# Performance work log

Measured on AMD Instinct MI355X. Metric: run time of the kernel, lower is better.

Reference implementation:

```python
import jax, jax.numpy as jnp
import numpy as np

B, CQ, CKV, H, W = 16, 512, 512, 48, 48
NH = 8
HD = CQ // NH
SCALE = HD ** -0.5


def setup_inputs() -> dict:
    key = jax.random.key(0)
    ks = jax.random.split(key, 11)
    s = 0.02
    return {
        "query_features": jax.random.normal(ks[0], (B, CQ, H, W), jnp.float32),
        "key_features": jax.random.normal(ks[1], (B, CKV, H, W), jnp.float32),
        "value_features": jax.random.normal(ks[2], (B, CKV, H, W), jnp.float32),
        "Wq": jax.random.normal(ks[3], (CQ, CQ), jnp.float32) * s,
        "bq": jnp.zeros((CQ,), jnp.float32),
        "Wk": jax.random.normal(ks[4], (CQ, CKV), jnp.float32) * s,
        "bk": jnp.zeros((CQ,), jnp.float32),
        "Wv": jax.random.normal(ks[5], (CQ, CKV), jnp.float32) * s,
        "bv": jnp.zeros((CQ,), jnp.float32),
        "Wo": jax.random.normal(ks[6], (CQ, CQ), jnp.float32) * s,
        "bo": jnp.zeros((CQ,), jnp.float32),
    }


def _proj(x, Wt, b):
    # 1x1 conv == channel GEMM: (O,C) x (B,C,H,W) -> (B,O,H,W)
    return jnp.einsum('oc,bchw->bohw', Wt, x) + b[None, :, None, None]


def reference(query_features, key_features, value_features,
              Wq, bq, Wk, bk, Wv, bv, Wo, bo):
    b, cq, h, w = query_features.shape
    hw = h * w
    Q = _proj(query_features, Wq, bq).reshape(b, NH, HD, hw)
    K = _proj(key_features, Wk, bk).reshape(b, NH, HD, hw)
    V = _proj(value_features, Wv, bv).reshape(b, NH, HD, hw)
    # NOTE: faithful to source — contraction is over the SPATIAL axis d=H*W,
    # so scores are (B, NH, HD, HD) (head_dim x head_dim attention).
    scores = jnp.einsum('bnhd,bnkd->bnhk', Q, K) * SCALE
    attn = jax.nn.softmax(scores, axis=-1)
    out = jnp.einsum('bnhk,bnkd->bnhd', attn, V)  # (B, NH, HD, HW)
    out = out.reshape(b, cq, h, w)
    return _proj(out, Wo, bo)
```

## Files before the change

### kernel.cpp

```cpp
#include <hip/hip_runtime.h>
#include <hip/hip_bf16.h>

#define B_   16
#define C_   512
#define HW_  2304
#define NH_  8
#define HD_  64
#define SCALE_ 0.125f

typedef __bf16 bf16x8 __attribute__((ext_vector_type(8)));
typedef __bf16 bf16x4 __attribute__((ext_vector_type(4)));
typedef float  f32x4  __attribute__((ext_vector_type(4)));

#define MFMA16(a, b, c) __builtin_amdgcn_mfma_f32_16x16x32_bf16((a), (b), (c), 0, 0, 0)

__device__ __forceinline__ void gload_lds16(const void* g, void* l) {
    __builtin_amdgcn_global_load_lds(
        (const __attribute__((address_space(1))) unsigned int*)g,
        (__attribute__((address_space(3))) unsigned int*)l, 16, 0, 0);
}

__global__ __launch_bounds__(256) void prep(
    const float* __restrict__ X, __bf16* __restrict__ XT,
    const float* __restrict__ W, __bf16* __restrict__ Wb)
{
    const int t = threadIdx.x;
    if (blockIdx.z == 16) {
        const int bid = blockIdx.y * 18 + blockIdx.x;
        if (bid < 128) {
            const int idx = bid * 2048 + t * 8;
            const float4 f0 = *(const float4*)&W[idx];
            const float4 f1 = *(const float4*)&W[idx + 4];
            bf16x8 o;
            o[0] = (__bf16)f0.x; o[1] = (__bf16)f0.y; o[2] = (__bf16)f0.z; o[3] = (__bf16)f0.w;
            o[4] = (__bf16)f1.x; o[5] = (__bf16)f1.y; o[6] = (__bf16)f1.z; o[7] = (__bf16)f1.w;
            *(bf16x8*)&Wb[idx] = o;
        }
        return;
    }
    const int b  = blockIdx.z;
    const int c0 = blockIdx.y * 64;
    const int h0 = blockIdx.x * 128;
    const float* Xb = X + (size_t)b * C_ * HW_;
    __bf16* XTb = XT + (size_t)b * HW_ * C_;

    __shared__ float Ts[64 * 129];

    #pragma unroll
    for (int p = 0; p < 8; ++p) {
        const int c  = p * 8 + (t >> 5);
        const int hg = (t & 31) * 4;
        const float4 v = *(const float4*)&Xb[(size_t)(c0 + c) * HW_ + h0 + hg];
        Ts[c * 129 + hg + 0] = v.x;
        Ts[c * 129 + hg + 1] = v.y;
        Ts[c * 129 + hg + 2] = v.z;
        Ts[c * 129 + hg + 3] = v.w;
    }
    __syncthreads();
    #pragma unroll
    for (int p = 0; p < 4; ++p) {
        const int hw = p * 32 + (t >> 3);
        const int g  = (t & 7) * 8;
        bf16x8 o;
        #pragma unroll
        for (int e = 0; e < 8; ++e)
            o[e] = (__bf16)Ts[(g + e) * 129 + hw];
        *(bf16x8*)&XTb[(size_t)(h0 + hw) * C_ + c0 + g] = o;
    }
}

template <typename OUT_T>
__device__ __forceinline__ void gemm_body(
    const __bf16* __restrict__ XTb, const __bf16* __restrict__ Wb,
    const float* __restrict__ bias, OUT_T* __restrict__ Yb,
    int n0, int m0)
{
    __shared__ __align__(16) __bf16 As[128 * 64];
    __shared__ __align__(16) __bf16 Bs[128 * 64];

    const int t = threadIdx.x;
    const int w = t >> 6, lane = t & 63, l16 = lane & 15, q = lane >> 4;
    const int wm = w >> 1, wn = w & 1;
    const int sr = lane >> 3;
    const int sg = ((lane & 7) ^ (lane >> 3)) * 8;

    f32x4 acc[4][4] = {};

    for (int ks = 0; ks < 8; ++ks) {
        const int k0 = ks * 64;
        __syncthreads();
        #pragma unroll
        for (int p = 0; p < 4; ++p) {
            const int rb = p * 32 + w * 8;
            gload_lds16(&Wb [(size_t)(m0 + rb + sr) * C_ + k0 + sg], &As[rb * 64]);
            gload_lds16(&XTb[(size_t)(n0 + rb + sr) * C_ + k0 + sg], &Bs[rb * 64]);
        }
        __syncthreads();
        #pragma unroll
        for (int kk = 0; kk < 2; ++kk) {
            const int sw = ((kk * 4 + q) ^ (l16 & 7)) * 8;
            bf16x8 af[4], bfr[4];
            #pragma unroll
            for (int mi = 0; mi < 4; ++mi)
                af[mi] = *(bf16x8*)&As[(wm * 64 + mi * 16 + l16) * 64 + sw];
            #pragma unroll
            for (int ni = 0; ni < 4; ++ni)
                bfr[ni] = *(bf16x8*)&Bs[(wn * 64 + ni * 16 + l16) * 64 + sw];
            #pragma unroll
            for (int mi = 0; mi < 4; ++mi)
                #pragma unroll
                for (int ni = 0; ni < 4; ++ni)
                    acc[mi][ni] = MFMA16(af[mi], bfr[ni], acc[mi][ni]);
        }
    }

    #pragma unroll
    for (int mi = 0; mi < 4; ++mi) {
        #pragma unroll
        for (int r = 0; r < 4; ++r) {
            const int m = m0 + wm * 64 + mi * 16 + q * 4 + r;
            const float bv_ = bias[m];
            #pragma unroll
            for (int ni = 0; ni < 4; ++ni) {
                const int n = n0 + wn * 64 + ni * 16 + l16;
                Yb[(size_t)m * HW_ + n] = (OUT_T)(acc[mi][ni][r] + bv_);
            }
        }
    }
}

__global__ __launch_bounds__(256) void proj_gemm(
    const __bf16* __restrict__ XT, const __bf16* __restrict__ Wb,
    const float* __restrict__ bias, __bf16* __restrict__ Y)
{
    const int b = blockIdx.z;
    gemm_body<__bf16>(XT + (size_t)b * HW_ * C_, Wb, bias,
                      Y + (size_t)b * C_ * HW_, blockIdx.x * 128, blockIdx.y * 128);
}

__global__ __launch_bounds__(256) void proj_out(
    const __bf16* __restrict__ AOT, const __bf16* __restrict__ Wb,
    const float* __restrict__ bias, float* __restrict__ out)
{
    const int b = blockIdx.z;
    gemm_body<float>(AOT + (size_t)b * HW_ * C_, Wb, bias,
                     out + (size_t)b * C_ * HW_, blockIdx.x * 128, blockIdx.y * 128);
}

__global__ __launch_bounds__(256) void attn_scores_part(
    const __bf16* __restrict__ Qw, const __bf16* __restrict__ Kw,
    float* __restrict__ Sp)
{
    const int bn  = blockIdx.x;
    const int kcs = blockIdx.y;
    const __bf16* Qb = Qw + (size_t)bn * 64 * HW_;
    const __bf16* Kb = Kw + (size_t)bn * 64 * HW_;

    __shared__ __align__(16) __bf16 Qs[64 * 64];
    __shared__ __align__(16) __bf16 Ks[64 * 64];

    const int t    = threadIdx.x;
    const int w    = t >> 6;
    const int lane = t & 63;
    const int l16  = lane & 15;
    const int q    = lane >> 4;
    const int sr   = lane >> 3;
    const int sg   = ((lane & 7) ^ (lane >> 3)) * 8;

    f32x4 acc[4] = {};

    for (int it = 0; it < 9; ++it) {
        const int k0 = kcs * 576 + it * 64;
        __syncthreads();
        #pragma unroll
        for (int p = 0; p < 2; ++p) {
            const int rb = w * 16 + p * 8;
            gload_lds16(&Qb[(size_t)(rb + sr) * HW_ + k0 + sg], &Qs[rb * 64]);
            gload_lds16(&Kb[(size_t)(rb + sr) * HW_ + k0 + sg], &Ks[rb * 64]);
        }
        __syncthreads();
        #pragma unroll
        for (int kk = 0; kk < 2; ++kk) {
            const int sw = ((kk * 4 + q) ^ (l16 & 7)) * 8;
            const bf16x8 a = *(bf16x8*)&Qs[(w * 16 + l16) * 64 + sw];
            #pragma unroll
            for (int ni = 0; ni < 4; ++ni) {
                const bf16x8 bb = *(bf16x8*)&Ks[(ni * 16 + l16) * 64 + sw];
                acc[ni] = MFMA16(a, bb, acc[ni]);
            }
        }
    }

    float* S = Sp + ((size_t)kcs * 128 + bn) * 4096;
    #pragma unroll
    for (int r = 0; r < 4; ++r)
        #pragma unroll
        for (int ni = 0; ni < 4; ++ni)
            S[(w * 16 + q * 4 + r) * 64 + ni * 16 + l16] = acc[ni][r];
}

__global__ __launch_bounds__(256) void softmax_reduce(
    const float* __restrict__ Sp, __bf16* __restrict__ Pw)
{
    const int bn = blockIdx.x;
    const int t  = threadIdx.x;
    const int r  = t >> 2;
    const int c0 = (t & 3) * 16;

    float v[16];
    #pragma unroll
    for (int j = 0; j < 16; ++j) v[j] = 0.f;
    #pragma unroll
    for (int kc = 0; kc < 4; ++kc) {
        const float* s = Sp + ((size_t)kc * 128 + bn) * 4096 + r * 64 + c0;
        #pragma unroll
        for (int j4 = 0; j4 < 4; ++j4) {
            const float4 f = *(const float4*)&s[j4 * 4];
            v[j4 * 4 + 0] += f.x; v[j4 * 4 + 1] += f.y;
            v[j4 * 4 + 2] += f.z; v[j4 * 4 + 3] += f.w;
        }
    }
    float mx = -1e30f;
    #pragma unroll
    for (int j = 0; j < 16; ++j) { v[j] *= SCALE_; mx = fmaxf(mx, v[j]); }
    mx = fmaxf(mx, __shfl_xor(mx, 1));
    mx = fmaxf(mx, __shfl_xor(mx, 2));
    float s = 0.f;
    #pragma unroll
    for (int j = 0; j < 16; ++j) { v[j] = __expf(v[j] - mx); s += v[j]; }
    s += __shfl_xor(s, 1);
    s += __shfl_xor(s, 2);
    const float inv = 1.f / s;
    bf16x8 o0, o1;
    #pragma unroll
    for (int j = 0; j < 8; ++j) {
        o0[j] = (__bf16)(v[j] * inv);
        o1[j] = (__bf16)(v[8 + j] * inv);
    }
    *(bf16x8*)&Pw[(size_t)bn * 4096 + r * 64 + c0]     = o0;
    *(bf16x8*)&Pw[(size_t)bn * 4096 + r * 64 + c0 + 8] = o1;
}

__global__ __launch_bounds__(256) void attn_pv(
    const __bf16* __restrict__ Pw, const __bf16* __restrict__ Vw,
    __bf16* __restrict__ AOT, const float* __restrict__ Wo, __bf16* __restrict__ WoB)
{
    const int t = threadIdx.x;
    if (blockIdx.x == 9) {
        const int idx = blockIdx.y * 2048 + t * 8;
        const float4 f0 = *(const float4*)&Wo[idx];
        const float4 f1 = *(const float4*)&Wo[idx + 4];
        bf16x8 o;
        o[0] = (__bf16)f0.x; o[1] = (__bf16)f0.y; o[2] = (__bf16)f0.z; o[3] = (__bf16)f0.w;
        o[4] = (__bf16)f1.x; o[5] = (__bf16)f1.y; o[6] = (__bf16)f1.z; o[7] = (__bf16)f1.w;
        *(bf16x8*)&WoB[idx] = o;
        return;
    }
    const int dsl = blockIdx.x;
    const int bn  = blockIdx.y;
    const int w    = t >> 6;
    const int lane = t & 63;
    const int l16  = lane & 15;
    const int q    = lane >> 4;

    __shared__ __align__(16) __bf16 Ps[64 * 72];
    __shared__ __align__(16) __bf16 Vt[4][16 * 264];

    {
        const int row = t >> 2;
        const int kc  = (t & 3) * 16;
        *(bf16x8*)&Ps[row * 72 + kc]     = *(const bf16x8*)&Pw[(size_t)bn * 4096 + row * 64 + kc];
        *(bf16x8*)&Ps[row * 72 + kc + 8] = *(const bf16x8*)&Pw[(size_t)bn * 4096 + row * 64 + kc + 8];
    }

    const __bf16* Vb = Vw + (size_t)bn * 64 * HW_;
    const int d0w = dsl * 256 + w * 64;
    {
        const int m4 = lane & 15;
        const int kh = (lane >> 4) * 16;
        __bf16 rr[4][16];
        #pragma unroll
        for (int j = 0; j < 16; ++j) {
            const bf16x4 v = *(const bf16x4*)&Vb[(size_t)(kh + j) * HW_ + d0w + 4 * m4];
            #pragma unroll
            for (int e = 0; e < 4; ++e) rr[e][j] = v[e];
        }
        #pragma unroll
        for (int e = 0; e < 4; ++e) {
            bf16x8 s0, s1;
            #pragma unroll
            for (int j = 0; j < 8; ++j) { s0[j] = rr[e][j]; s1[j] = rr[e][8 + j]; }
            *(bf16x8*)&Vt[w][m4 * 264 + e * 64 + kh]     = s0;
            *(bf16x8*)&Vt[w][m4 * 264 + e * 64 + kh + 8] = s1;
        }
    }
    __syncthreads();

    f32x4 acc[4][4] = {};
    #pragma unroll
    for (int kk = 0; kk < 2; ++kk) {
        bf16x8 af[4], bfr[4];
        #pragma unroll
        for (int mi = 0; mi < 4; ++mi)
            af[mi] = *(bf16x8*)&Ps[(mi * 16 + l16) * 72 + kk * 32 + q * 8];
        #pragma unroll
        for (int ni = 0; ni < 4; ++ni) {
            const int dl = ni * 16 + l16;
            bfr[ni] = *(bf16x8*)&Vt[w][(dl >> 2) * 264 + (dl & 3) * 64 + kk * 32 + q * 8];
        }
        #pragma unroll
        for (int mi = 0; mi < 4; ++mi)
            #pragma unroll
            for (int ni = 0; ni < 4; ++ni)
                acc[mi][ni] = MFMA16(af[mi], bfr[ni], acc[mi][ni]);
    }

    const int bb = bn >> 3;
    const int nh = bn & 7;
    #pragma unroll
    for (int mi = 0; mi < 4; ++mi)
        #pragma unroll
        for (int ni = 0; ni < 4; ++ni) {
            const int d = d0w + ni * 16 + l16;
            bf16x4 o;
            #pragma unroll
            for (int r = 0; r < 4; ++r) o[r] = (__bf16)acc[mi][ni][r];
            *(bf16x4*)&AOT[((size_t)bb * HW_ + d) * C_ + nh * 64 + mi * 16 + q * 4] = o;
        }
}

extern "C" void kernel_launch(void* const* d_in, const int* in_sizes, int n_in,
                              void* d_out, int out_size, void* d_ws, size_t ws_size,
                              hipStream_t stream)
{
    (void)in_sizes; (void)n_in; (void)out_size; (void)ws_size;
    const float* qf = (const float*)d_in[0];
    const float* kf = (const float*)d_in[1];
    const float* vf = (const float*)d_in[2];
    const float* Wq = (const float*)d_in[3];
    const float* bq = (const float*)d_in[4];
    const float* Wk = (const float*)d_in[5];
    const float* bk = (const float*)d_in[6];
    const float* Wv = (const float*)d_in[7];
    const float* bv = (const float*)d_in[8];
    const float* Wo = (const float*)d_in[9];
    const float* bo = (const float*)d_in[10];

    const size_t QE = (size_t)B_ * C_ * HW_;
    __bf16* region0 = (__bf16*)d_ws;
    __bf16* XT  = region0;
    float*  Sp  = (float*)region0;
    __bf16* AOT = region0;
    __bf16* Qw  = region0 + QE;
    __bf16* Kw  = Qw + QE;
    __bf16* Vw  = Kw + QE;
    __bf16* slotP = Vw + QE;
    __bf16* Wb  = slotP;
    __bf16* Pw  = slotP;
    __bf16* WoB = Qw;

    prep     <<<dim3(18, 8, 17), 256, 0, stream>>>(qf, XT, Wq, Wb);
    proj_gemm<<<dim3(18, 4, 16), 256, 0, stream>>>(XT, Wb, bq, Qw);
    prep     <<<dim3(18, 8, 17), 256, 0, stream>>>(kf, XT, Wk, Wb);
    proj_gemm<<<dim3(18, 4, 16), 256, 0, stream>>>(XT, Wb, bk, Kw);
    prep     <<<dim3(18, 8, 17), 256, 0, stream>>>(vf, XT, Wv, Wb);
    proj_gemm<<<dim3(18, 4, 16), 256, 0, stream>>>(XT, Wb, bv, Vw);

    attn_scores_part<<<dim3(128, 4), 256, 0, stream>>>(Qw, Kw, Sp);
    softmax_reduce  <<<dim3(128),    256, 0, stream>>>(Sp, Pw);
    attn_pv         <<<dim3(10, 128), 256, 0, stream>>>(Pw, Vw, AOT, Wo, WoB);
    proj_out        <<<dim3(18, 4, 16), 256, 0, stream>>>(AOT, WoB, bo, (float*)d_out);
}
```

Baseline: 424.8 us.

## Batch Q/K/V prep and projection GEMMs into single launches, store V transposed

Merges the three prep launches and three projection GEMM launches into one prep and one gemm_all kernel, with a wider grid that fills the GPU better and needs fewer launches. The V projection now writes its output transposed (spatial-major), so attn_pv can load V tiles straight into LDS with global_load_lds instead of transposing them in registers. The score split goes from 4 to 6 chunks, and all four weight conversions move into prep. To fit the larger workspace, d_out is reused as scratch for the transposed Q/K inputs, which depends on proj_out running last.

```diff
diff --git a/kernel.cpp b/kernel.cpp
--- a/kernel.cpp
+++ b/kernel.cpp
@@ -21,36 +21,47 @@
 }
 
 __global__ __launch_bounds__(256) void prep(
-    const float* __restrict__ X, __bf16* __restrict__ XT,
-    const float* __restrict__ W, __bf16* __restrict__ Wb)
+    const float* __restrict__ qf, const float* __restrict__ kf, const float* __restrict__ vf,
+    __bf16* __restrict__ XTq, __bf16* __restrict__ XTk, __bf16* __restrict__ XTv,
+    const float* __restrict__ Wq, const float* __restrict__ Wk,
+    const float* __restrict__ Wv, const float* __restrict__ Wo,
+    __bf16* __restrict__ Wb)
 {
     const int t = threadIdx.x;
-    if (blockIdx.z == 16) {
+    if (blockIdx.z == 48) {
         const int bid = blockIdx.y * 18 + blockIdx.x;
         if (bid < 128) {
-            const int idx = bid * 2048 + t * 8;
-            const float4 f0 = *(const float4*)&W[idx];
-            const float4 f1 = *(const float4*)&W[idx + 4];
-            bf16x8 o;
-            o[0] = (__bf16)f0.x; o[1] = (__bf16)f0.y; o[2] = (__bf16)f0.z; o[3] = (__bf16)f0.w;
-            o[4] = (__bf16)f1.x; o[5] = (__bf16)f1.y; o[6] = (__bf16)f1.z; o[7] = (__bf16)f1.w;
-            *(bf16x8*)&Wb[idx] = o;
+            const int wsel = bid >> 5;
+            const float* W = (wsel == 0) ? Wq : (wsel == 1) ? Wk : (wsel == 2) ? Wv : Wo;
+            __bf16* D = Wb + wsel * 262144;
+            const int off = (bid & 31) * 8192 + t * 32;
+            #pragma unroll
+            for (int c = 0; c < 4; ++c) {
+                const float4 f0 = *(const float4*)&W[off + c * 8];
+                const float4 f1 = *(const float4*)&W[off + c * 8 + 4];
+                bf16x8 o;
+                o[0] = (__bf16)f0.x; o[1] = (__bf16)f0.y; o[2] = (__bf16)f0.z; o[3] = (__bf16)f0.w;
+                o[4] = (__bf16)f1.x; o[5] = (__bf16)f1.y; o[6] = (__bf16)f1.z; o[7] = (__bf16)f1.w;
+                *(bf16x8*)&D[off + c * 8] = o;
+            }
         }
         return;
     }
-    const int b  = blockIdx.z;
+    const int p = blockIdx.z >> 4;
+    const int b = blockIdx.z & 15;
+    const float* X = ((p == 0) ? qf : (p == 1) ? kf : vf) + (size_t)b * C_ * HW_;
+    __bf16* XT = ((p == 0) ? XTq : (p == 1) ? XTk : XTv) + (size_t)b * HW_ * C_;
+
     const int c0 = blockIdx.y * 64;
     const int h0 = blockIdx.x * 128;
-    const float* Xb = X + (size_t)b * C_ * HW_;
-    __bf16* XTb = XT + (size_t)b * HW_ * C_;
 
     __shared__ float Ts[64 * 129];
 
     #pragma unroll
-    for (int p = 0; p < 8; ++p) {
-        const int c  = p * 8 + (t >> 5);
+    for (int pp = 0; pp < 8; ++pp) {
+        const int c  = pp * 8 + (t >> 5);
         const int hg = (t & 31) * 4;
-        const float4 v = *(const float4*)&Xb[(size_t)(c0 + c) * HW_ + h0 + hg];
+        const float4 v = *(const float4*)&X[(size_t)(c0 + c) * HW_ + h0 + hg];
         Ts[c * 129 + hg + 0] = v.x;
         Ts[c * 129 + hg + 1] = v.y;
         Ts[c * 129 + hg + 2] = v.z;
@@ -58,22 +69,22 @@
     }
     __syncthreads();
     #pragma unroll
-    for (int p = 0; p < 4; ++p) {
-        const int hw = p * 32 + (t >> 3);
+    for (int pp = 0; pp < 4; ++pp) {
+        const int hw = pp * 32 + (t >> 3);
         const int g  = (t & 7) * 8;
         bf16x8 o;
         #pragma unroll
         for (int e = 0; e < 8; ++e)
             o[e] = (__bf16)Ts[(g + e) * 129 + hw];
-        *(bf16x8*)&XTb[(size_t)(h0 + hw) * C_ + c0 + g] = o;
-    }
-}
-
-template <typename OUT_T>
-__device__ __forceinline__ void gemm_body(
-    const __bf16* __restrict__ XTb, const __bf16* __restrict__ Wb,
-    const float* __restrict__ bias, OUT_T* __restrict__ Yb,
-    int n0, int m0)
+        *(bf16x8*)&XT[(size_t)(h0 + hw) * C_ + c0 + g] = o;
+    }
+}
+
+template <bool BIAS_N, typename OUT_T>
+__device__ __forceinline__ void gemm_core(
+    const __bf16* __restrict__ A, const __bf16* __restrict__ Bm,
+    const float* __restrict__ bias, OUT_T* __restrict__ Y, int ldY,
+    int m0, int n0)
 {
     __shared__ __align__(16) __bf16 As[128 * 64];
     __shared__ __align__(16) __bf16 Bs[128 * 64];
@@ -92,8 +103,8 @@
         #pragma unroll
         for (int p = 0; p < 4; ++p) {
             const int rb = p * 32 + w * 8;
-            gload_lds16(&Wb [(size_t)(m0 + rb + sr) * C_ + k0 + sg], &As[rb * 64]);
-            gload_lds16(&XTb[(size_t)(n0 + rb + sr) * C_ + k0 + sg], &Bs[rb * 64]);
+            gload_lds16(&A [(size_t)(m0 + rb + sr) * C_ + k0 + sg], &As[rb * 64]);
+            gload_lds16(&Bm[(size_t)(n0 + rb + sr) * C_ + k0 + sg], &Bs[rb * 64]);
         }
         __syncthreads();
         #pragma unroll
@@ -114,37 +125,52 @@
         }
     }
 
+    float bnv[4];
+    if (BIAS_N) {
+        #pragma unroll
+        for (int ni = 0; ni < 4; ++ni)
+            bnv[ni] = bias[n0 + wn * 64 + ni * 16 + l16];
+    }
     #pragma unroll
     for (int mi = 0; mi < 4; ++mi) {
         #pragma unroll
         for (int r = 0; r < 4; ++r) {
             const int m = m0 + wm * 64 + mi * 16 + q * 4 + r;
-            const float bv_ = bias[m];
+            const float bm = BIAS_N ? 0.f : bias[m];
             #pragma unroll
             for (int ni = 0; ni < 4; ++ni) {
                 const int n = n0 + wn * 64 + ni * 16 + l16;
-                Yb[(size_t)m * HW_ + n] = (OUT_T)(acc[mi][ni][r] + bv_);
+                const float v = acc[mi][ni][r] + (BIAS_N ? bnv[ni] : bm);
+                Y[(size_t)m * ldY + n] = (OUT_T)v;
             }
         }
     }
 }
 
-__global__ __launch_bounds__(256) void proj_gemm(
-    const __bf16* __restrict__ XT, const __bf16* __restrict__ Wb,
-    const float* __restrict__ bias, __bf16* __restrict__ Y)
-{
-    const int b = blockIdx.z;
-    gemm_body<__bf16>(XT + (size_t)b * HW_ * C_, Wb, bias,
-                      Y + (size_t)b * C_ * HW_, blockIdx.x * 128, blockIdx.y * 128);
-}
-
-__global__ __launch_bounds__(256) void proj_out(
-    const __bf16* __restrict__ AOT, const __bf16* __restrict__ Wb,
-    const float* __restrict__ bias, float* __restrict__ out)
-{
-    const int b = blockIdx.z;
-    gemm_body<float>(AOT + (size_t)b * HW_ * C_, Wb, bias,
-                     out + (size_t)b * C_ * HW_, blockIdx.x * 128, blockIdx.y * 128);
+__global__ __launch_bounds__(256) void gemm_all(
+    const __bf16* __restrict__ XTq, const __bf16* __restrict__ XTk,
+    const __bf16* __restrict__ XTv, const __bf16* __restrict__ Wb,
+    const float* __restrict__ bq, const float* __restrict__ bk,
+    const float* __restrict__ bv,
+    __bf16* __restrict__ Qw, __bf16* __restrict__ Kw, __bf16* __restrict__ VTw)
+{
+    const int x = blockIdx.x;
+    const int p = blockIdx.y >> 4;
+    const int b = blockIdx.y & 15;
+    if (p == 2) {
+        const int m0 = (x % 18) * 128;
+        const int n0 = (x / 18) * 128;
+        gemm_core<true, __bf16>(XTv + (size_t)b * HW_ * C_, Wb + 2 * 262144,
+                                bv, VTw + (size_t)b * HW_ * C_, C_, m0, n0);
+    } else {
+        const int m0 = (x & 3) * 128;
+        const int n0 = (x >> 2) * 128;
+        const __bf16* XT = (p == 0) ? XTq : XTk;
+        __bf16* Y = (p == 0) ? Qw : Kw;
+        gemm_core<false, __bf16>(Wb + p * 262144, XT + (size_t)b * HW_ * C_,
+                                 (p == 0) ? bq : bk,
+                                 Y + (size_t)b * C_ * HW_, HW_, m0, n0);
+    }
 }
 
 __global__ __launch_bounds__(256) void attn_scores_part(
@@ -169,8 +195,8 @@
 
     f32x4 acc[4] = {};
 
-    for (int it = 0; it < 9; ++it) {
-        const int k0 = kcs * 576 + it * 64;
+    for (int it = 0; it < 6; ++it) {
+        const int k0 = kcs * 384 + it * 64;
         __syncthreads();
         #pragma unroll
         for (int p = 0; p < 2; ++p) {
@@ -211,7 +237,7 @@
     #pragma unroll
     for (int j = 0; j < 16; ++j) v[j] = 0.f;
     #pragma unroll
-    for (int kc = 0; kc < 4; ++kc) {
+    for (int kc = 0; kc < 6; ++kc) {
         const float* s = Sp + ((size_t)kc * 128 + bn) * 4096 + r * 64 + c0;
         #pragma unroll
         for (int j4 = 0; j4 < 4; ++j4) {
@@ -242,72 +268,48 @@
 }
 
 __global__ __launch_bounds__(256) void attn_pv(
-    const __bf16* __restrict__ Pw, const __bf16* __restrict__ Vw,
-    __bf16* __restrict__ AOT, const float* __restrict__ Wo, __bf16* __restrict__ WoB)
-{
-    const int t = threadIdx.x;
-    if (blockIdx.x == 9) {
-        const int idx = blockIdx.y * 2048 + t * 8;
-        const float4 f0 = *(const float4*)&Wo[idx];
-        const float4 f1 = *(const float4*)&Wo[idx + 4];
-        bf16x8 o;
-        o[0] = (__bf16)f0.x; o[1] = (__bf16)f0.y; o[2] = (__bf16)f0.z; o[3] = (__bf16)f0.w;
-        o[4] = (__bf16)f1.x; o[5] = (__bf16)f1.y; o[6] = (__bf16)f1.z; o[7] = (__bf16)f1.w;
-        *(bf16x8*)&WoB[idx] = o;
-        return;
-    }
+    const __bf16* __restrict__ Pw, const __bf16* __restrict__ VTw,
+    __bf16* __restrict__ AOT)
+{
     const int dsl = blockIdx.x;
     const int bn  = blockIdx.y;
+    const int bb  = bn >> 3;
+    const int nh  = bn & 7;
+    const int t    = threadIdx.x;
     const int w    = t >> 6;
     const int lane = t & 63;
     const int l16  = lane & 15;
     const int q    = lane >> 4;
-
-    __shared__ __align__(16) __bf16 Ps[64 * 72];
-    __shared__ __align__(16) __bf16 Vt[4][16 * 264];
-
-    {
-        const int row = t >> 2;
-        const int kc  = (t & 3) * 16;
-        *(bf16x8*)&Ps[row * 72 + kc]     = *(const bf16x8*)&Pw[(size_t)bn * 4096 + row * 64 + kc];
-        *(bf16x8*)&Ps[row * 72 + kc + 8] = *(const bf16x8*)&Pw[(size_t)bn * 4096 + row * 64 + kc + 8];
-    }
-
-    const __bf16* Vb = Vw + (size_t)bn * 64 * HW_;
-    const int d0w = dsl * 256 + w * 64;
-    {
-        const int m4 = lane & 15;
-        const int kh = (lane >> 4) * 16;
-        __bf16 rr[4][16];
-        #pragma unroll
-        for (int j = 0; j < 16; ++j) {
-            const bf16x4 v = *(const bf16x4*)&Vb[(size_t)(kh + j) * HW_ + d0w + 4 * m4];
-            #pragma unroll
-            for (int e = 0; e < 4; ++e) rr[e][j] = v[e];
-        }
-        #pragma unroll
-        for (int e = 0; e < 4; ++e) {
-            bf16x8 s0, s1;
-            #pragma unroll
-            for (int j = 0; j < 8; ++j) { s0[j] = rr[e][j]; s1[j] = rr[e][8 + j]; }
-            *(bf16x8*)&Vt[w][m4 * 264 + e * 64 + kh]     = s0;
-            *(bf16x8*)&Vt[w][m4 * 264 + e * 64 + kh + 8] = s1;
-        }
+    const int sr   = lane >> 3;
+    const int sg   = ((lane & 7) ^ (lane >> 3)) * 8;
+
+    __shared__ __align__(16) __bf16 Ps[64 * 64];
+    __shared__ __align__(16) __bf16 Vs[256 * 64];
+
+    #pragma unroll
+    for (int p = 0; p < 2; ++p) {
+        const int rb = w * 16 + p * 8;
+        gload_lds16(&Pw[(size_t)bn * 4096 + (rb + sr) * 64 + sg], &Ps[rb * 64]);
+    }
+    const __bf16* Vbase = VTw + ((size_t)bb * HW_ + dsl * 256) * C_ + nh * 64;
+    #pragma unroll
+    for (int p = 0; p < 8; ++p) {
+        const int rb = w * 64 + p * 8;
+        gload_lds16(&Vbase[(size_t)(rb + sr) * C_ + sg], &Vs[rb * 64]);
     }
     __syncthreads();
 
     f32x4 acc[4][4] = {};
     #pragma unroll
     for (int kk = 0; kk < 2; ++kk) {
+        const int sw = ((kk * 4 + q) ^ (l16 & 7)) * 8;
         bf16x8 af[4], bfr[4];
         #pragma unroll
         for (int mi = 0; mi < 4; ++mi)
-            af[mi] = *(bf16x8*)&Ps[(mi * 16 + l16) * 72 + kk * 32 + q * 8];
-        #pragma unroll
-        for (int ni = 0; ni < 4; ++ni) {
-            const int dl = ni * 16 + l16;
-            bfr[ni] = *(bf16x8*)&Vt[w][(dl >> 2) * 264 + (dl & 3) * 64 + kk * 32 + q * 8];
-        }
+            af[mi] = *(bf16x8*)&Ps[(mi * 16 + l16) * 64 + sw];
+        #pragma unroll
+        for (int ni = 0; ni < 4; ++ni)
+            bfr[ni] = *(bf16x8*)&Vs[(w * 64 + ni * 16 + l16) * 64 + sw];
         #pragma unroll
         for (int mi = 0; mi < 4; ++mi)
             #pragma unroll
@@ -315,18 +317,28 @@
                 acc[mi][ni] = MFMA16(af[mi], bfr[ni], acc[mi][ni]);
     }
 
-    const int bb = bn >> 3;
-    const int nh = bn & 7;
     #pragma unroll
     for (int mi = 0; mi < 4; ++mi)
         #pragma unroll
         for (int ni = 0; ni < 4; ++ni) {
-            const int d = d0w + ni * 16 + l16;
+            const int d = dsl * 256 + w * 64 + ni * 16 + l16;
             bf16x4 o;
             #pragma unroll
             for (int r = 0; r < 4; ++r) o[r] = (__bf16)acc[mi][ni][r];
             *(bf16x4*)&AOT[((size_t)bb * HW_ + d) * C_ + nh * 64 + mi * 16 + q * 4] = o;
         }
+}
+
+__global__ __launch_bounds__(256) void proj_out(
+    const __bf16* __restrict__ AOT, const __bf16* __restrict__ WoB,
+    const float* __restrict__ bo, float* __restrict__ out)
+{
+    const int x = blockIdx.x;
+    const int b = blockIdx.y;
+    const int m0 = (x & 3) * 128;
+    const int n0 = (x >> 2) * 128;
+    gemm_core<false, float>(WoB, AOT + (size_t)b * HW_ * C_, bo,
+                            out + (size_t)b * C_ * HW_, HW_, m0, n0);
 }
 
 extern "C" void kernel_launch(void* const* d_in, const int* in_sizes, int n_in,
@@ -347,27 +359,25 @@
     const float* bo = (const float*)d_in[10];
 
     const size_t QE = (size_t)B_ * C_ * HW_;
-    __bf16* region0 = (__bf16*)d_ws;
-    __bf16* XT  = region0;
-    float*  Sp  = (float*)region0;
-    __bf16* AOT = region0;
-    __bf16* Qw  = region0 + QE;
-    __bf16* Kw  = Qw + QE;
-    __bf16* Vw  = Kw + QE;
-    __bf16* slotP = Vw + QE;
-    __bf16* Wb  = slotP;
-    __bf16* Pw  = slotP;
-    __bf16* WoB = Qw;
-
-    prep     <<<dim3(18, 8, 17), 256, 0, stream>>>(qf, XT, Wq, Wb);
-    proj_gemm<<<dim3(18, 4, 16), 256, 0, stream>>>(XT, Wb, bq, Qw);
-    prep     <<<dim3(18, 8, 17), 256, 0, stream>>>(kf, XT, Wk, Wb);
-    proj_gemm<<<dim3(18, 4, 16), 256, 0, stream>>>(XT, Wb, bk, Kw);
-    prep     <<<dim3(18, 8, 17), 256, 0, stream>>>(vf, XT, Wv, Wb);
-    proj_gemm<<<dim3(18, 4, 16), 256, 0, stream>>>(XT, Wb, bv, Vw);
-
-    attn_scores_part<<<dim3(128, 4), 256, 0, stream>>>(Qw, Kw, Sp);
-    softmax_reduce  <<<dim3(128),    256, 0, stream>>>(Sp, Pw);
-    attn_pv         <<<dim3(10, 128), 256, 0, stream>>>(Pw, Vw, AOT, Wo, WoB);
-    proj_out        <<<dim3(18, 4, 16), 256, 0, stream>>>(AOT, WoB, bo, (float*)d_out);
-}
+    __bf16* XTq = (__bf16*)d_out;
+    __bf16* XTk = XTq + QE;
+    __bf16* base = (__bf16*)d_ws;
+    __bf16* XTv = base;
+    float*  Sp  = (float*)base;
+    __bf16* AOT = base;
+    __bf16* Qw  = base + QE;
+    __bf16* Kw  = base + 2 * QE;
+    __bf16* VTw = base + 3 * QE;
+    __bf16* Wb  = base + 4 * QE;
+    __bf16* Pw  = Wb + 4 * 262144;
+
+    prep            <<<dim3(18, 8, 49), 256, 0, stream>>>(qf, kf, vf, XTq, XTk, XTv,
+                                                          Wq, Wk, Wv, Wo, Wb);
+    gemm_all        <<<dim3(72, 48),    256, 0, stream>>>(XTq, XTk, XTv, Wb,
+                                                          bq, bk, bv, Qw, Kw, VTw);
+    attn_scores_part<<<dim3(128, 6),    256, 0, stream>>>(Qw, Kw, Sp);
+    softmax_reduce  <<<dim3(128),       256, 0, stream>>>(Sp, Pw);
+    attn_pv         <<<dim3(9, 128),    256, 0, stream>>>(Pw, VTw, AOT);
+    proj_out        <<<dim3(72, 16),    256, 0, stream>>>(AOT, Wb + 3 * 262144, bo,
+                                                          (float*)d_out);
+}
```

New measurement: 475.3 us. +11.9%, slower.
